# Kernel optimization log

Measured on AMD Instinct MI355X. Metric: run time of the kernel, lower is better.

## Reference

```python
import jax, jax.numpy as jnp
import numpy as np

N, F_IN, T, E, O = 50000, 32, 8, 800000, 32


def setup_inputs() -> dict:
    ks = jax.random.split(jax.random.key(0), 16)
    s = 0.05
    return {
        "X": jax.random.normal(ks[0], (N, F_IN, T), dtype=jnp.float32),
        "edge_index": jax.random.randint(ks[1], (2, E), 0, N, dtype=jnp.int64),
        "edge_weight": jax.random.uniform(ks[2], (E,), dtype=jnp.float32),
        # GCNConv weights for z/r/h gates: lin weight [O, F_IN], bias [O]
        "Wz": jax.random.normal(ks[3], (O, F_IN), dtype=jnp.float32) * s,
        "bz": jnp.zeros((O,), dtype=jnp.float32),
        "Wr": jax.random.normal(ks[4], (O, F_IN), dtype=jnp.float32) * s,
        "br": jnp.zeros((O,), dtype=jnp.float32),
        "Wh": jax.random.normal(ks[5], (O, F_IN), dtype=jnp.float32) * s,
        "bh": jnp.zeros((O,), dtype=jnp.float32),
        # Linear(2*O, O) per gate
        "Lz": jax.random.normal(ks[6], (O, 2 * O), dtype=jnp.float32) * s,
        "lz_b": jnp.zeros((O,), dtype=jnp.float32),
        "Lr": jax.random.normal(ks[7], (O, 2 * O), dtype=jnp.float32) * s,
        "lr_b": jnp.ones((O,), dtype=jnp.float32),
        "Lh": jax.random.normal(ks[8], (O, 2 * O), dtype=jnp.float32) * s,
        "lh_b": jnp.zeros((O,), dtype=jnp.float32),
        "attention": jax.random.uniform(ks[9], (T,), dtype=jnp.float32),
    }


def reference(X, edge_index, edge_weight, Wz, bz, Wr, br, Wh, bh,
              Lz, lz_b, Lr, lr_b, Lh, lh_b, attention):
    n = X.shape[0]
    # --- GCN normalization with self-loops (computed once; graph is static) ---
    loop = jnp.arange(n, dtype=edge_index.dtype)
    row = jnp.concatenate([edge_index[0], loop])
    col = jnp.concatenate([edge_index[1], loop])
    ew = jnp.concatenate([edge_weight, jnp.ones((n,), dtype=X.dtype)])
    deg = jax.ops.segment_sum(ew, col, num_segments=n)
    deg_safe = jnp.where(deg > 0, deg, 1.0)
    dinv = jnp.where(deg > 0, jax.lax.rsqrt(deg_safe), 0.0)
    norm = dinv[row] * ew * dinv[col]  # [E+N]

    def conv(x, W, b):
        h = x @ W.T                                   # [N, O]
        msg = norm[:, None] * h[row]                  # gather over sources
        return jax.ops.segment_sum(msg, col, num_segments=n) + b

    def tgcn_cell(x, H):
        Z = jax.nn.sigmoid(jnp.concatenate([conv(x, Wz, bz), H], axis=1) @ Lz.T + lz_b)
        R = jax.nn.sigmoid(jnp.concatenate([conv(x, Wr, br), H], axis=1) @ Lr.T + lr_b)
        H_tilde = jnp.tanh(jnp.concatenate([conv(x, Wh, bh), H * R], axis=1) @ Lh.T + lh_b)
        return Z * H + (1.0 - Z) * H_tilde

    H0 = jnp.zeros((n, Lz.shape[0]), dtype=X.dtype)   # hidden init (H=None)
    probs = jax.nn.softmax(attention)
    Xs = jnp.moveaxis(X, 2, 0)                        # [T, N, F]

    def step(acc, inp):
        x_t, p = inp
        return acc + p * tgcn_cell(x_t, H0), None

    H_accum, _ = jax.lax.scan(step, H0, (Xs, probs))
    return H_accum
```

## Files before the change

kernel.cpp:

```cpp
#include <hip/hip_runtime.h>
#include <hip/hip_fp16.h>
#include <math.h>


#define GATH16(EV, WT)                                                     \
  {                                                                        \
    unsigned voff = ((unsigned)(EV) << 9) | loff;                          \
    uint2 q = *(const uint2*)((const char*)Xh + voff);                     \
    __half2 ha = *(__half2*)&q.x;                                          \
    __half2 hb = *(__half2*)&q.y;                                          \
    acc.x = fmaf((WT), __low2float(ha),  acc.x);                           \
    acc.y = fmaf((WT), __high2float(ha), acc.y);                           \
    acc.z = fmaf((WT), __low2float(hb),  acc.z);                           \
    acc.w = fmaf((WT), __high2float(hb), acc.w);                           \
  }

__device__ inline void do_prep(int g, int tid,
    const float* __restrict__ Wz, const float* __restrict__ bz,
    const float* __restrict__ Wh, const float* __restrict__ bh,
    const float* __restrict__ Lz, const float* __restrict__ lzb,
    const float* __restrict__ Lh, const float* __restrict__ lhb,
    const float* __restrict__ att,
    float* __restrict__ Mt, float* __restrict__ cvec, float* __restrict__ p) {
  const float* L  = g ? Lh  : Lz;
  const float* W  = g ? Wh  : Wz;
  const float* bb = g ? bh  : bz;
  const float* lb = g ? lhb : lzb;
  int o = tid & 31;
  for (int f = tid >> 5; f < 32; f += 8) {
    float s = 0.f;
    for (int k = 0; k < 32; ++k) s += L[o * 64 + k] * W[k * 32 + f];
    Mt[g * 1024 + f * 32 + o] = s;
  }
  if (tid < 32) {
    float c = lb[tid];
    for (int k = 0; k < 32; ++k) c += L[tid * 64 + k] * bb[k];
    cvec[g * 32 + tid] = c;
  }
  if (g == 0 && tid == 0) {
    float m = att[0];
    for (int t = 1; t < 8; ++t) m = fmaxf(m, att[t]);
    float e8[8], sm = 0.f;
    for (int t = 0; t < 8; ++t) { e8[t] = expf(att[t] - m); sm += e8[t]; }
    for (int t = 0; t < 8; ++t) p[t] = e8[t] / sm;
  }
}

__global__ __launch_bounds__(256) void kA(
    const float* __restrict__ X, const int* __restrict__ ei,
    const float* __restrict__ ew, unsigned long long* __restrict__ pk,
    int2* __restrict__ slot, int cap, __half* __restrict__ Xh,
    const float* __restrict__ Wz, const float* __restrict__ bz,
    const float* __restrict__ Wh, const float* __restrict__ bh,
    const float* __restrict__ Lz, const float* __restrict__ lzb,
    const float* __restrict__ Lh, const float* __restrict__ lhb,
    const float* __restrict__ att,
    float* __restrict__ Mt, float* __restrict__ cvec, float* __restrict__ p,
    int E, long n8, int nbe4) {
  int b = blockIdx.x;
  int tid = threadIdx.x;
  if (b < 2) { do_prep(b, tid, Wz, bz, Wh, bh, Lz, lzb, Lh, lhb, att, Mt, cvec, p); return; }
  b -= 2;
  if (b < nbe4) {
    int base = b * 1024 + tid;
#pragma unroll
    for (int k = 0; k < 4; ++k) {
      int e = base + k * 256;
      if (e < E) {
        int r = ei[e];
        int c = ei[E + e];
        float w = ew[e];
        unsigned wfx = (unsigned)(w * 16777216.0f + 0.5f);
        unsigned long long old =
            atomicAdd(pk + c, ((unsigned long long)wfx << 32) | 1ull);
        unsigned pos = (unsigned)(old & 0xffffffffull);
        if (pos < (unsigned)cap)
          slot[(size_t)c * cap + pos] = make_int2(r, __float_as_int(w));
      }
    }
    return;
  }
  b -= nbe4;
  long i = (long)b * 256 + tid;
  if (i < n8) {
    const float4* Xv = (const float4*)X;
    float4 a = Xv[2 * i], c = Xv[2 * i + 1];
    union { int4 i4; __half2 h[4]; } u;
    u.h[0] = __floats2half2_rn(a.x, a.y);
    u.h[1] = __floats2half2_rn(a.z, a.w);
    u.h[2] = __floats2half2_rn(c.x, c.y);
    u.h[3] = __floats2half2_rn(c.z, c.w);
    ((int4*)Xh)[i] = u.i4;
  }
}

__global__ __launch_bounds__(64) void kD(
    const unsigned long long* __restrict__ pk, int2* __restrict__ slot,
    int cap) {
  int node = blockIdx.x;
  int l = threadIdx.x;
  unsigned long long v = pk[node];
  int cnt = (int)(v & 0xffffffffull);
  if (cnt > cap) cnt = cap;
  if (l < cnt) {
    size_t idx = (size_t)node * cap + l;
    int2 s = slot[idx];
    unsigned long long pv = pk[s.x];
    float dis = rsqrtf((float)(pv >> 32) * (1.0f / 16777216.0f) + 1.0f);
    s.y = __float_as_int(__int_as_float(s.y) * dis);
    slot[idx] = s;
  }
}

__global__ __launch_bounds__(64) void k3_main(
    const __half* __restrict__ Xh, const unsigned long long* __restrict__ pk,
    const int2* __restrict__ slot, int cap,
    const float* __restrict__ Mt, const float* __restrict__ cvec,
    const float* __restrict__ p, float* __restrict__ out) {
  int node = blockIdx.x;
  int l = threadIdx.x;
  __shared__ float ax[256];

  unsigned long long v = pk[node];
  int cnt = (int)(v & 0xffffffffull);
  if (cnt > cap) cnt = cap;
  float di = rsqrtf((float)(v >> 32) * (1.0f / 16777216.0f) + 1.0f);

  float4 acc = make_float4(0.f, 0.f, 0.f, 0.f);
  unsigned loff = (unsigned)l << 3;

  GATH16(node, di);
  const int2* row = slot + (size_t)node * cap;
  int j = 0;
  for (; j + 7 < cnt; j += 8) {
    int2 e0 = row[j],     e1 = row[j + 1], e2 = row[j + 2], e3 = row[j + 3];
    int2 e4 = row[j + 4], e5 = row[j + 5], e6 = row[j + 6], e7 = row[j + 7];
    GATH16(e0.x, __int_as_float(e0.y));
    GATH16(e1.x, __int_as_float(e1.y));
    GATH16(e2.x, __int_as_float(e2.y));
    GATH16(e3.x, __int_as_float(e3.y));
    GATH16(e4.x, __int_as_float(e4.y));
    GATH16(e5.x, __int_as_float(e5.y));
    GATH16(e6.x, __int_as_float(e6.y));
    GATH16(e7.x, __int_as_float(e7.y));
  }
  for (; j < cnt; ++j) {
    int2 e0 = row[j];
    GATH16(e0.x, __int_as_float(e0.y));
  }
  acc.x *= di; acc.y *= di; acc.z *= di; acc.w *= di;

  ((float4*)ax)[l] = acc;
  __syncthreads();

  int o = l & 31, g = l >> 5;
  float c = cvec[g * 32 + o];
  float pre[8];
#pragma unroll
  for (int t = 0; t < 8; ++t) pre[t] = c;

  const float*  M   = Mt + g * 1024;
  const float4* axv = (const float4*)ax;
#pragma unroll 8
  for (int f = 0; f < 32; ++f) {
    float  m  = M[f * 32 + o];
    float4 a0 = axv[f * 2];
    float4 a1 = axv[f * 2 + 1];
    pre[0] = fmaf(m, a0.x, pre[0]); pre[1] = fmaf(m, a0.y, pre[1]);
    pre[2] = fmaf(m, a0.z, pre[2]); pre[3] = fmaf(m, a0.w, pre[3]);
    pre[4] = fmaf(m, a1.x, pre[4]); pre[5] = fmaf(m, a1.y, pre[5]);
    pre[6] = fmaf(m, a1.z, pre[6]); pre[7] = fmaf(m, a1.w, pre[7]);
  }

  float vv[8];
  if (g == 0) {
#pragma unroll
    for (int t = 0; t < 8; ++t)
      vv[t] = __builtin_amdgcn_rcpf(1.f + __expf(pre[t]));
  } else {
#pragma unroll
    for (int t = 0; t < 8; ++t)
      vv[t] = 1.f - 2.f * __builtin_amdgcn_rcpf(__expf(2.f * pre[t]) + 1.f);
  }

  float res = 0.f;
#pragma unroll
  for (int t = 0; t < 8; ++t) {
    float other = __shfl(vv[t], l ^ 32);
    res += p[t] * vv[t] * other;
  }
  if (g == 0) out[(size_t)node * 32 + o] = res;
}


extern "C" void kernel_launch(void* const* d_in, const int* in_sizes, int n_in,
                              void* d_out, int out_size, void* d_ws, size_t ws_size,
                              hipStream_t stream) {
  const float* X   = (const float*)d_in[0];
  const int*   ei  = (const int*)d_in[1];
  const float* ew  = (const float*)d_in[2];
  const float* Wz  = (const float*)d_in[3];
  const float* bz  = (const float*)d_in[4];
  const float* Wh  = (const float*)d_in[7];
  const float* bh  = (const float*)d_in[8];
  const float* Lz  = (const float*)d_in[9];
  const float* lzb = (const float*)d_in[10];
  const float* Lh  = (const float*)d_in[13];
  const float* lhb = (const float*)d_in[14];
  const float* att = (const float*)d_in[15];

  int N = in_sizes[0] / 256;
  int E = in_sizes[2];
  (void)n_in; (void)out_size;

  long n8   = (long)N * 32;
  int  nbe4 = (E + 1023) / 1024;
  int  nbc  = (int)((n8 + 255) / 256);

  size_t off = 0;
  auto al = [&](size_t b) { size_t q = off; off = (off + b + 255) & ~(size_t)255; return q; };
  size_t o_pk  = al((size_t)N * 8);
  size_t o_mt  = al(2048 * 4);
  size_t o_cv  = al(64 * 4);
  size_t o_p   = al(8 * 4);
  size_t o_xh  = al((size_t)N * 256 * 2);
  size_t fixed = off;
  int cap = 0;
  for (int c : {64, 48, 32}) {
    if (fixed + (size_t)N * c * 8 <= ws_size) { cap = c; break; }
  }
  if (!cap) return;

  char* w = (char*)d_ws;
  unsigned long long* pk = (unsigned long long*)(w + o_pk);
  float* Mt   = (float*)(w + o_mt);
  float* cvec = (float*)(w + o_cv);
  float* p    = (float*)(w + o_p);
  __half* Xh  = (__half*)(w + o_xh);
  int2*  slot = (int2*)(w + fixed);

  (void)hipMemsetAsync(pk, 0, (size_t)N * 8, stream);
  kA<<<2 + nbe4 + nbc, 256, 0, stream>>>(X, ei, ew, pk, slot, cap, Xh,
                                         Wz, bz, Wh, bh, Lz, lzb, Lh, lhb,
                                         att, Mt, cvec, p, E, n8, nbe4);
  kD<<<N, 64, 0, stream>>>(pk, slot, cap);
  k3_main<<<N, 64, 0, stream>>>(Xh, pk, slot, cap, Mt, cvec, p,
                                (float*)d_out);
}
```

Baseline: 139.2 us.

## Fold source-degree scaling into half-precision X and partition edge scatter by destination

Removes the per-edge weight renormalization kernel. The source-side rsqrt(deg) factor is now applied during the fp32-to-fp16 conversion of X, which becomes its own kernel placed after the degree counts are final. The edge bucketing kernel is also split into 8 destination-range partitions: each block reads the destination index of every edge in its stride but only inserts edges in its slice, meant to localize atomics and slot writes. The cost is reading the edge column 8 times and losing the overlap between edge bucketing and X conversion.

```diff
diff --git a/kernel.cpp b/kernel.cpp
--- a/kernel.cpp
+++ b/kernel.cpp
@@ -46,69 +46,60 @@
   }
 }
 
-__global__ __launch_bounds__(256) void kA(
-    const float* __restrict__ X, const int* __restrict__ ei,
-    const float* __restrict__ ew, unsigned long long* __restrict__ pk,
-    int2* __restrict__ slot, int cap, __half* __restrict__ Xh,
+__global__ __launch_bounds__(256) void k1_part(
+    const int* __restrict__ ei, const float* __restrict__ ew,
+    unsigned long long* __restrict__ pk, int2* __restrict__ slot, int cap,
     const float* __restrict__ Wz, const float* __restrict__ bz,
     const float* __restrict__ Wh, const float* __restrict__ bh,
     const float* __restrict__ Lz, const float* __restrict__ lzb,
     const float* __restrict__ Lh, const float* __restrict__ lhb,
     const float* __restrict__ att,
     float* __restrict__ Mt, float* __restrict__ cvec, float* __restrict__ p,
-    int E, long n8, int nbe4) {
+    int E, int N, int K) {
   int b = blockIdx.x;
   int tid = threadIdx.x;
-  if (b < 2) { do_prep(b, tid, Wz, bz, Wh, bh, Lz, lzb, Lh, lhb, att, Mt, cvec, p); return; }
-  b -= 2;
-  if (b < nbe4) {
-    int base = b * 1024 + tid;
-#pragma unroll
-    for (int k = 0; k < 4; ++k) {
-      int e = base + k * 256;
-      if (e < E) {
-        int r = ei[e];
-        int c = ei[E + e];
-        float w = ew[e];
-        unsigned wfx = (unsigned)(w * 16777216.0f + 0.5f);
-        unsigned long long old =
-            atomicAdd(pk + c, ((unsigned long long)wfx << 32) | 1ull);
-        unsigned pos = (unsigned)(old & 0xffffffffull);
-        if (pos < (unsigned)cap)
-          slot[(size_t)c * cap + pos] = make_int2(r, __float_as_int(w));
-      }
+  int nedge = K << 3;
+  if (b >= nedge) {
+    do_prep(b - nedge, tid, Wz, bz, Wh, bh, Lz, lzb, Lh, lhb, att, Mt, cvec, p);
+    return;
+  }
+  int g = b & 7;
+  int n = b >> 3;
+  int slice = (N + 7) >> 3;
+  int lo = g * slice;
+  int hi = lo + slice; if (hi > N) hi = N;
+  int stride = K << 8;
+  for (int e = (n << 8) + tid; e < E; e += stride) {
+    int c = ei[E + e];
+    if (c >= lo && c < hi) {
+      int r = ei[e];
+      float w = ew[e];
+      unsigned wfx = (unsigned)(w * 16777216.0f + 0.5f);
+      unsigned long long old =
+          atomicAdd(pk + c, ((unsigned long long)wfx << 32) | 1ull);
+      unsigned pos = (unsigned)(old & 0xffffffffull);
+      if (pos < (unsigned)cap)
+        slot[(size_t)c * cap + pos] = make_int2(r, __float_as_int(w));
     }
-    return;
-  }
-  b -= nbe4;
-  long i = (long)b * 256 + tid;
+  }
+}
+
+__global__ __launch_bounds__(256) void k2_conv(
+    const float* __restrict__ X, const unsigned long long* __restrict__ pk,
+    __half* __restrict__ Xh, long n8) {
+  long i = blockIdx.x * (long)blockDim.x + threadIdx.x;
   if (i < n8) {
+    int node = (int)(i >> 5);
+    unsigned long long v = pk[node];
+    float di = rsqrtf((float)(v >> 32) * (1.0f / 16777216.0f) + 1.0f);
     const float4* Xv = (const float4*)X;
     float4 a = Xv[2 * i], c = Xv[2 * i + 1];
     union { int4 i4; __half2 h[4]; } u;
-    u.h[0] = __floats2half2_rn(a.x, a.y);
-    u.h[1] = __floats2half2_rn(a.z, a.w);
-    u.h[2] = __floats2half2_rn(c.x, c.y);
-    u.h[3] = __floats2half2_rn(c.z, c.w);
+    u.h[0] = __floats2half2_rn(di * a.x, di * a.y);
+    u.h[1] = __floats2half2_rn(di * a.z, di * a.w);
+    u.h[2] = __floats2half2_rn(di * c.x, di * c.y);
+    u.h[3] = __floats2half2_rn(di * c.z, di * c.w);
     ((int4*)Xh)[i] = u.i4;
-  }
-}
-
-__global__ __launch_bounds__(64) void kD(
-    const unsigned long long* __restrict__ pk, int2* __restrict__ slot,
-    int cap) {
-  int node = blockIdx.x;
-  int l = threadIdx.x;
-  unsigned long long v = pk[node];
-  int cnt = (int)(v & 0xffffffffull);
-  if (cnt > cap) cnt = cap;
-  if (l < cnt) {
-    size_t idx = (size_t)node * cap + l;
-    int2 s = slot[idx];
-    unsigned long long pv = pk[s.x];
-    float dis = rsqrtf((float)(pv >> 32) * (1.0f / 16777216.0f) + 1.0f);
-    s.y = __float_as_int(__int_as_float(s.y) * dis);
-    slot[idx] = s;
   }
 }
 
@@ -129,7 +120,7 @@
   float4 acc = make_float4(0.f, 0.f, 0.f, 0.f);
   unsigned loff = (unsigned)l << 3;
 
-  GATH16(node, di);
+  GATH16(node, 1.0f);
   const int2* row = slot + (size_t)node * cap;
   int j = 0;
   for (; j + 7 < cnt; j += 8) {
@@ -213,9 +204,9 @@
   int E = in_sizes[2];
   (void)n_in; (void)out_size;
 
-  long n8   = (long)N * 32;
-  int  nbe4 = (E + 1023) / 1024;
-  int  nbc  = (int)((n8 + 255) / 256);
+  long n8  = (long)N * 32;
+  int  nbc = (int)((n8 + 255) / 256);
+  int  K   = (E + 2047) / 2048;
 
   size_t off = 0;
   auto al = [&](size_t b) { size_t q = off; off = (off + b + 255) & ~(size_t)255; return q; };
@@ -240,10 +231,10 @@
   int2*  slot = (int2*)(w + fixed);
 
   (void)hipMemsetAsync(pk, 0, (size_t)N * 8, stream);
-  kA<<<2 + nbe4 + nbc, 256, 0, stream>>>(X, ei, ew, pk, slot, cap, Xh,
+  k1_part<<<K * 8 + 2, 256, 0, stream>>>(ei, ew, pk, slot, cap,
                                          Wz, bz, Wh, bh, Lz, lzb, Lh, lhb,
-                                         att, Mt, cvec, p, E, n8, nbe4);
-  kD<<<N, 64, 0, stream>>>(pk, slot, cap);
+                                         att, Mt, cvec, p, E, N, K);
+  k2_conv<<<nbc, 256, 0, stream>>>(X, pk, Xh, n8);
   k3_main<<<N, 64, 0, stream>>>(Xh, pk, slot, cap, Mt, cvec, p,
                                 (float*)d_out);
 }
```

Measured after the change: 126.5 us (median of 2 runs). -9.1%, faster.
